# Performance work log

Hardware: AMD Instinct MI355X
Metric: run time of the kernel (lower is better)

Reference implementation:

```python
import jax, jax.numpy as jnp
import numpy as np

# dims
B, S, E, H = 2, 2048, 2048, 2688   # batch, seq, embedding_dim, hidden_dim
NH, DH = 4, 2688 // 4              # mLSTM heads, head dim
KS = 4                             # causal conv kernel size
BLK = 4                            # qkv_proj_blocksize
NPH = H // BLK                     # headwise-proj heads


def setup_inputs() -> dict:
    key = jax.random.key(0)
    ks = jax.random.split(key, 12)
    r = lambda i, shape, s=0.02: jax.random.normal(ks[i], shape, jnp.float32) * s
    return dict(
        x=jax.random.normal(ks[0], (B, S, E), jnp.float32),
        W_in=r(1, (E, 2 * H)),                       # up projection (no bias)
        conv_w=r(2, (KS, 1, H), 0.1),                # depthwise causal conv kernel (W, I/g, O)
        conv_b=jnp.zeros((H,), jnp.float32),
        Wq=r(3, (NPH, BLK, BLK), 0.3),               # headwise q proj
        Wk=r(4, (NPH, BLK, BLK), 0.3),               # headwise k proj
        Wv=r(5, (NPH, BLK, BLK), 0.3),               # headwise v proj
        W_ig=r(6, (3 * H, NH)),                      # input gate proj
        b_ig=jax.random.normal(ks[7], (NH,), jnp.float32),
        W_fg=r(8, (3 * H, NH)),                      # forget gate proj
        b_fg=jnp.linspace(3.0, 6.0, NH).astype(jnp.float32),
        norm_w=jnp.ones((H,), jnp.float32),          # multi-head layernorm weight
        skip=jnp.ones((H,), jnp.float32),            # learnable skip
        W_out=r(9, (H, E)),                          # down projection
    )


def _headwise(x, W):
    # LinearHeadwiseExpand: (B,S,H) -> (B,S,NPH,BLK) -> einsum -> (B,S,H)
    b, s, _ = x.shape
    xh = x.reshape(b, s, NPH, BLK)
    return jnp.einsum('bshd,hdo->bsho', xh, W).reshape(b, s, -1)


def reference(x, W_in, conv_w, conv_b, Wq, Wk, Wv, W_ig, b_ig, W_fg, b_fg, norm_w, skip, W_out):
    x_inner = x @ W_in                               # (B,S,2H)
    x_m, z = jnp.split(x_inner, 2, axis=-1)
    # depthwise causal conv1d
    xc = jax.lax.conv_general_dilated(
        x_m, conv_w, (1,), [(KS - 1, 0)],
        dimension_numbers=('NWC', 'WIO', 'NWC'), feature_group_count=H) + conv_b
    xca = jax.nn.silu(xc)
    q = _headwise(xca, Wq)
    k = _headwise(xca, Wk)
    v = _headwise(x_m, Wv)
    # ---- mLSTM cell (parallel stabilized form) ----
    qh = q.reshape(B, S, NH, DH).transpose(0, 2, 1, 3)   # (B,NH,S,DH)
    kh = k.reshape(B, S, NH, DH).transpose(0, 2, 1, 3)
    vh = v.reshape(B, S, NH, DH).transpose(0, 2, 1, 3)
    if_in = jnp.concatenate([q, k, v], axis=-1)          # (B,S,3H)
    i_pre = (if_in @ W_ig + b_ig).transpose(0, 2, 1)     # (B,NH,S)
    f_pre = (if_in @ W_fg + b_fg).transpose(0, 2, 1)
    log_fg = jax.nn.log_sigmoid(f_pre)                   # (B,NH,S)
    cs = jnp.cumsum(log_fg, axis=-1)
    # log decay matrix: sum of log forget gates t=j+1..i, causal masked
    dmat = cs[:, :, :, None] - cs[:, :, None, :]         # (B,NH,S,S)
    mask = jnp.tril(jnp.ones((S, S), bool))
    log_D = jnp.where(mask, dmat + i_pre[:, :, None, :], -jnp.inf)
    m = jnp.max(log_D, axis=-1, keepdims=True)           # stabilizer (B,NH,S,1)
    D = jnp.exp(log_D - m)
    qk = jnp.einsum('bnsd,bntd->bnst', qh, kh) / jnp.sqrt(jnp.float32(DH))
    C = qk * D
    n = jnp.maximum(jnp.abs(C.sum(-1, keepdims=True)), jnp.exp(-m))
    h = jnp.einsum('bnst,bntd->bnsd', C / (n + 1e-6), vh)
    # multi-head layernorm over DH, learnable scale over full H
    mu = h.mean(-1, keepdims=True)
    var = h.var(-1, keepdims=True)
    hn = (h - mu) * jax.lax.rsqrt(var + 1e-5)
    hn = hn.transpose(0, 2, 1, 3).reshape(B, S, H) * norm_w
    # ---- gated skip + output ----
    h_skip = hn + skip * xca
    hs = h_skip * jax.nn.silu(z)
    return hs @ W_out
```

## Files before the change

### kernel.cpp

```cpp
#include <hip/hip_runtime.h>

typedef unsigned short u16;
typedef unsigned int u32;
typedef __bf16 bf16x8 __attribute__((ext_vector_type(8)));
typedef float f32x4 __attribute__((ext_vector_type(4)));

#define BB   2
#define SS   2048
#define EE   2048
#define HH   2688
#define NHH  4
#define DHH  672
#define NPHH 672
#define H2   5376
#define H3   8064

__device__ __forceinline__ float b2f(u16 u) {
  union { unsigned int i; float f; } c; c.i = ((unsigned int)u) << 16; return c.f;
}
__device__ __forceinline__ u16 f2b(float f) {
  union { float f; unsigned int i; } c; c.f = f;
  unsigned int i = c.i;
  return (u16)((i + 0x7FFFu + ((i >> 16) & 1u)) >> 16);
}
__device__ __forceinline__ float silu_f(float x) { return x / (1.f + __expf(-x)); }
__device__ __forceinline__ float logsig_f(float f) {
  return (f >= 0.f) ? -log1pf(__expf(-f)) : (f - log1pf(__expf(f)));
}

__device__ __forceinline__ void gl2lds16(const u16* g, u16* s) {
  __builtin_amdgcn_global_load_lds(
      (const __attribute__((address_space(1))) u32*)g,
      (__attribute__((address_space(3))) u32*)s, 16, 0, 0);
}

template <int MODE, int OUTF32>
__global__ __launch_bounds__(256) void gemm_nt(
    const u16* __restrict__ A, const u16* __restrict__ Bt, void* __restrict__ Cp,
    int M, int N, int K, int lda, int ldb, int ldc,
    long sAhi, long sAlo, long sBhi, long sBlo, long sChi, long sClo,
    const float* __restrict__ aux1, const float* __restrict__ aux2,
    int auxStride, int causal)
{
  __shared__ __align__(16) u16 As[128 * 32];
  __shared__ __align__(16) u16 Bs[128 * 32];
  int m0 = blockIdx.y * 128, n0 = blockIdx.x * 128;
  if (MODE == 1 && n0 > m0 + 127) return;
  int bz = blockIdx.z, bzh = bz >> 2, bzl = bz & 3;
  A  += bzh * sAhi + bzl * sAlo;
  Bt += bzh * sBhi + bzl * sBlo;
  const float* a1 = aux1 ? aux1 + (long)bz * auxStride : nullptr;
  const float* a2 = aux2 ? aux2 + (long)bz * auxStride : nullptr;
  u16*   C16 = (u16*)Cp + bzh * sChi + bzl * sClo;
  float* C32 = (float*)Cp + bzh * sChi + bzl * sClo;

  int t = threadIdx.x, lane = t & 63, wid = t >> 6;
  int wm = (wid >> 1) * 64, wn = (wid & 1) * 64;
  int l15 = lane & 15, quad = lane >> 4;

  int srow = wid * 16 + (lane >> 2);
  int scol = (lane & 3) * 8;
  const u16* pA0 = A + (long)(m0 + srow) * lda + scol;
  const u16* pA1 = pA0 + (long)64 * lda;
  const u16* pB0 = Bt + (long)(n0 + srow) * ldb + scol;
  const u16* pB1 = pB0 + (long)64 * ldb;
  u16* dA = As + wid * 512;
  u16* dB = Bs + wid * 512;

  f32x4 acc[4][4];
#pragma unroll
  for (int i = 0; i < 4; i++)
#pragma unroll
    for (int j = 0; j < 4; j++) acc[i][j] = (f32x4){0.f, 0.f, 0.f, 0.f};

  int Keff = (MODE == 2 && causal) ? min(K, m0 + 128) : K;

  for (int k0 = 0; k0 < Keff; k0 += 32) {
    __syncthreads();
    gl2lds16(pA0 + k0, dA);
    gl2lds16(pA1 + k0, dA + 2048);
    gl2lds16(pB0 + k0, dB);
    gl2lds16(pB1 + k0, dB + 2048);
    __syncthreads();
    bf16x8 af[4], bfr[4];
#pragma unroll
    for (int i = 0; i < 4; i++) {
      af[i]  = *reinterpret_cast<const bf16x8*>(&As[(wm + i * 16 + l15) * 32 + quad * 8]);
      bfr[i] = *reinterpret_cast<const bf16x8*>(&Bs[(wn + i * 16 + l15) * 32 + quad * 8]);
    }
#pragma unroll
    for (int i = 0; i < 4; i++)
#pragma unroll
      for (int j = 0; j < 4; j++)
        acc[i][j] = __builtin_amdgcn_mfma_f32_16x16x32_bf16(af[i], bfr[j], acc[i][j], 0, 0, 0);
  }

  const float rs = 0.03857583749f;
#pragma unroll
  for (int i = 0; i < 4; i++) {
#pragma unroll
    for (int j = 0; j < 4; j++) {
      int col = n0 + wn + j * 16 + l15;
      if (col >= N) continue;
#pragma unroll
      for (int rr = 0; rr < 4; rr++) {
        int row = m0 + wm + i * 16 + quad * 4 + rr;
        if (row >= M) continue;
        float v = acc[i][j][rr];
        if (MODE == 1) v = (col <= row) ? v * rs * __expf(a1[col] - a2[row]) : 0.f;
        else if (MODE == 2) v = v * a1[row];
        if (OUTF32) C32[(long)row * ldc + col] = v;
        else        C16[(long)row * ldc + col] = f2b(v);
      }
    }
  }
}

template <int F32IN>
__global__ __launch_bounds__(256) void transpose_any(
    const void* __restrict__ in, u16* __restrict__ out, int R, int C, int ldin,
    long inHi, long inLo, long outStride)
{
  __shared__ u16 tile[64][65];
  int bz = blockIdx.z, bzh = bz >> 2, bzl = bz & 3;
  const u16* in16 = (const u16*)in + bzh * inHi + bzl * inLo;
  const float* inf = (const float*)in + bzh * inHi + bzl * inLo;
  out += (long)bz * outStride;
  int r0 = blockIdx.y * 64, c0 = blockIdx.x * 64;
  int t = threadIdx.x;
  for (int idx = t; idx < 64 * 64; idx += 256) {
    int r = idx >> 6, c = idx & 63;
    int rr = r0 + r, cc = c0 + c;
    u16 v = 0;
    if (rr < R && cc < C) {
      long off = (long)rr * ldin + cc;
      v = F32IN ? f2b(inf[off]) : in16[off];
    }
    tile[r][c] = v;
  }
  __syncthreads();
  for (int idx = t; idx < 64 * 64; idx += 256) {
    int r = idx & 63, c = idx >> 6;
    int rr = r0 + r, cc = c0 + c;
    if (rr < R && cc < C) out[(long)cc * R + rr] = tile[r][c];
  }
}

__global__ __launch_bounds__(256) void convert_x(
    const float* __restrict__ x, u16* __restrict__ o)
{
  long i = ((long)blockIdx.x * 256 + threadIdx.x) * 8;
  if (i >= (long)4096 * EE) return;
  float4 a = *reinterpret_cast<const float4*>(x + i);
  float4 b = *reinterpret_cast<const float4*>(x + i + 4);
  u16 t8[8] = {f2b(a.x), f2b(a.y), f2b(a.z), f2b(a.w),
               f2b(b.x), f2b(b.y), f2b(b.z), f2b(b.w)};
  *reinterpret_cast<uint4*>(o + i) = *reinterpret_cast<uint4*>(t8);
}

__global__ __launch_bounds__(256) void prep_wt3(
    const float* __restrict__ Wig, const float* __restrict__ Wfg,
    u16* __restrict__ WT3)
{
  int i = blockIdx.x * 256 + threadIdx.x;
  if (i >= 128 * HH) return;
  int r = i / HH, c = i % HH;
  float v = 0.f;
  if (r < 24) {
    int seg = r >> 3, j = r & 7;
    const float* W = (j < 4) ? Wig : Wfg;
    v = W[(long)(seg * HH + c) * 4 + (j & 3)];
  }
  WT3[i] = f2b(v);
}

__global__ __launch_bounds__(256) void prep_wqkv(
    const float* __restrict__ Wq, const float* __restrict__ Wk,
    const float* __restrict__ Wv, u16* __restrict__ o)
{
  int i = blockIdx.x * 256 + threadIdx.x;
  if (i >= 3 * 10752) return;
  int m = i / 10752, j = i % 10752;
  const float* W = (m == 0) ? Wq : (m == 1) ? Wk : Wv;
  o[i] = f2b(W[j]);
}

__global__ __launch_bounds__(256) void conv_silu(
    const u16* __restrict__ xinner, const float* __restrict__ cw,
    const float* __restrict__ cb, u16* __restrict__ xca)
{
  long idx = (long)blockIdx.x * 256 + threadIdx.x;
  if (idx >= (long)BB * SS * HH / 4) return;
  int h4 = (int)(idx % (HH / 4)) * 4;
  long bs = idx / (HH / 4);
  int s = (int)(bs % SS);
  float4 acc = *reinterpret_cast<const float4*>(cb + h4);
#pragma unroll
  for (int w = 0; w < 4; w++) {
    int sp = s + w - 3;
    if (sp < 0) continue;
    uint2 xr = *reinterpret_cast<const uint2*>(xinner + (bs + w - 3) * H2 + h4);
    const u16* xh = (const u16*)&xr;
    float4 cwv = *reinterpret_cast<const float4*>(cw + w * HH + h4);
    acc.x += b2f(xh[0]) * cwv.x;
    acc.y += b2f(xh[1]) * cwv.y;
    acc.z += b2f(xh[2]) * cwv.z;
    acc.w += b2f(xh[3]) * cwv.w;
  }
  u16 o4[4] = {f2b(silu_f(acc.x)), f2b(silu_f(acc.y)),
               f2b(silu_f(acc.z)), f2b(silu_f(acc.w))};
  *reinterpret_cast<uint2*>(xca + bs * HH + h4) = *reinterpret_cast<uint2*>(o4);
}

__global__ __launch_bounds__(256) void headwise_qkv(
    const u16* __restrict__ xinner, const u16* __restrict__ xca,
    const u16* __restrict__ Wqkv,
    u16* __restrict__ q, u16* __restrict__ k, u16* __restrict__ v)
{
  int idx = blockIdx.x * 256 + threadIdx.x;
  if (idx >= BB * SS * NPHH) return;
  int nph = idx % NPHH;
  long bs = idx / NPHH;
  int cbase = nph * 4;
  uint2 xar = *reinterpret_cast<const uint2*>(xca + bs * HH + cbase);
  uint2 xmr = *reinterpret_cast<const uint2*>(xinner + bs * H2 + cbase);
  const u16* xa = (const u16*)&xar;
  const u16* xm = (const u16*)&xmr;
  float xaf[4], xmf[4];
#pragma unroll
  for (int d = 0; d < 4; d++) { xaf[d] = b2f(xa[d]); xmf[d] = b2f(xm[d]); }
  union { uint4 v4[2]; u16 h[16]; } wq, wk, wv;
  const uint4* wqp = reinterpret_cast<const uint4*>(Wqkv + nph * 16);
  const uint4* wkp = reinterpret_cast<const uint4*>(Wqkv + 10752 + nph * 16);
  const uint4* wvp = reinterpret_cast<const uint4*>(Wqkv + 21504 + nph * 16);
  wq.v4[0] = wqp[0]; wq.v4[1] = wqp[1];
  wk.v4[0] = wkp[0]; wk.v4[1] = wkp[1];
  wv.v4[0] = wvp[0]; wv.v4[1] = wvp[1];
  u16 qo[4], ko[4], vo[4];
#pragma unroll
  for (int o = 0; o < 4; o++) {
    float aq = 0.f, ak = 0.f, av = 0.f;
#pragma unroll
    for (int d = 0; d < 4; d++) {
      aq += xaf[d] * b2f(wq.h[d * 4 + o]);
      ak += xaf[d] * b2f(wk.h[d * 4 + o]);
      av += xmf[d] * b2f(wv.h[d * 4 + o]);
    }
    qo[o] = f2b(aq); ko[o] = f2b(ak); vo[o] = f2b(av);
  }
  long ob = bs * HH + cbase;
  *reinterpret_cast<uint2*>(q + ob) = *reinterpret_cast<uint2*>(qo);
  *reinterpret_cast<uint2*>(k + ob) = *reinterpret_cast<uint2*>(ko);
  *reinterpret_cast<uint2*>(v + ob) = *reinterpret_cast<uint2*>(vo);
}

__global__ __launch_bounds__(1024) void scan_kernel(
    const float* __restrict__ G, const float* __restrict__ big,
    const float* __restrict__ bfg,
    float* __restrict__ avec, float* __restrict__ rmaxvec, float* __restrict__ mvec)
{
  __shared__ float buf[2][SS];
  __shared__ float isave[SS];
  __shared__ float cssave[SS];
  int bn = blockIdx.x;
  int b = bn >> 2, n = bn & 3;
  int t = threadIdx.x;
  float bi = big[n], bf = bfg[n];
  for (int i = t; i < SS; i += 1024) {
    long tk = (long)b * SS + i;
    float ip = G[tk * 24 + n] + G[(4096 + tk) * 24 + 8 + n] +
               G[(8192 + tk) * 24 + 16 + n] + bi;
    float fp = G[tk * 24 + 4 + n] + G[(4096 + tk) * 24 + 12 + n] +
               G[(8192 + tk) * 24 + 20 + n] + bf;
    isave[i] = ip;
    buf[0][i] = logsig_f(fp);
  }
  __syncthreads();
  int src = 0;
  for (int off = 1; off < SS; off <<= 1) {
    int dst = 1 - src;
    for (int i = t; i < SS; i += 1024) {
      float x = buf[src][i];
      if (i >= off) x += buf[src][i - off];
      buf[dst][i] = x;
    }
    __syncthreads();
    src = dst;
  }
  for (int i = t; i < SS; i += 1024) {
    float cs = buf[src][i];
    cssave[i] = cs;
    float a = isave[i] - cs;
    avec[(long)bn * SS + i] = a;
    buf[src][i] = a;
  }
  __syncthreads();
  for (int off = 1; off < SS; off <<= 1) {
    int dst = 1 - src;
    for (int i = t; i < SS; i += 1024) {
      float x = buf[src][i];
      if (i >= off) x = fmaxf(x, buf[src][i - off]);
      buf[dst][i] = x;
    }
    __syncthreads();
    src = dst;
  }
  for (int i = t; i < SS; i += 1024) {
    rmaxvec[(long)bn * SS + i] = buf[src][i];
    mvec[(long)bn * SS + i] = cssave[i] + buf[src][i];
  }
}

__global__ __launch_bounds__(256) void rowsum_kernel(
    const u16* __restrict__ P, const float* __restrict__ mvec, float* __restrict__ invn,
    long Pstride)
{
  int bz = blockIdx.z;
  P += (long)bz * Pstride;
  mvec += (long)bz * SS;
  invn += (long)bz * SS;
  int row = (blockIdx.x * 256 + threadIdx.x) >> 6;
  int lane = threadIdx.x & 63;
  if (row >= SS) return;
  const u16* pr = P + (long)row * SS;
  float s = 0.f;
  for (int j = lane; j <= row; j += 64) s += b2f(pr[j]);
#pragma unroll
  for (int off = 32; off > 0; off >>= 1) s += __shfl_down(s, off);
  if (lane == 0) {
    float n = fmaxf(fabsf(s), __expf(-mvec[row]));
    invn[row] = 1.f / (n + 1e-6f);
  }
}

__global__ __launch_bounds__(256) void ln_skip_gate(
    const u16* __restrict__ h, const u16* __restrict__ xca,
    const u16* __restrict__ xinner, const float* __restrict__ normw,
    const float* __restrict__ skipw, u16* __restrict__ hs)
{
  int row = (blockIdx.x * 256 + threadIdx.x) >> 6;
  int lane = threadIdx.x & 63;
  if (row >= BB * NHH * SS) return;
  int s = row % SS;
  int n = (row / SS) % NHH;
  int b = row / (SS * NHH);
  const u16* hr = h + (long)row * DHH;
  float sum = 0.f, ss = 0.f;
  float vals[11];
  int cnt = 0;
  for (int d = lane; d < DHH; d += 64) {
    float x = b2f(hr[d]);
    vals[cnt++] = x; sum += x; ss += x * x;
  }
#pragma unroll
  for (int off = 32; off > 0; off >>= 1) { sum += __shfl_down(sum, off); ss += __shfl_down(ss, off); }
  sum = __shfl(sum, 0); ss = __shfl(ss, 0);
  float mu = sum / (float)DHH;
  float var = ss / (float)DHH - mu * mu;
  float rstd = rsqrtf(var + 1e-5f);
  long bs = (long)b * SS + s;
  cnt = 0;
  for (int d = lane; d < DHH; d += 64) {
    int c = n * DHH + d;
    float hn = (vals[cnt++] - mu) * rstd * normw[c];
    float hskip = hn + skipw[c] * b2f(xca[bs * HH + c]);
    float z = b2f(xinner[bs * H2 + HH + c]);
    hs[bs * HH + c] = f2b(hskip * silu_f(z));
  }
}

__global__ __launch_bounds__(256) void fill_sentinel(float* out, float v, long n) {
  long i = (long)blockIdx.x * 256 + threadIdx.x;
  if (i < n) out[i] = v;
}

extern "C" void kernel_launch(void* const* d_in, const int* in_sizes, int n_in,
                              void* d_out, int out_size, void* d_ws, size_t ws_size,
                              hipStream_t stream)
{
  const float* x      = (const float*)d_in[0];
  const float* W_in   = (const float*)d_in[1];
  const float* conv_w = (const float*)d_in[2];
  const float* conv_b = (const float*)d_in[3];
  const float* Wq     = (const float*)d_in[4];
  const float* Wk     = (const float*)d_in[5];
  const float* Wv     = (const float*)d_in[6];
  const float* W_ig   = (const float*)d_in[7];
  const float* b_ig   = (const float*)d_in[8];
  const float* W_fg   = (const float*)d_in[9];
  const float* b_fg   = (const float*)d_in[10];
  const float* norm_w = (const float*)d_in[11];
  const float* skipw  = (const float*)d_in[12];
  const float* W_out  = (const float*)d_in[13];
  float* out = (float*)d_out;
  const long SD = (long)SS * DHH;
  const long SP = (long)SS * SS;
  const long BH = (long)SS * HH;

  u16* ws = (u16*)d_ws;
  size_t off = 0;
  auto alloc = [&](size_t n) { u16* p = ws + off; off += n; return p; };
  u16* x_inner = alloc((size_t)4096 * H2);
  u16* xca     = alloc((size_t)4096 * HH);
  u16* qb      = alloc((size_t)4096 * HH);
  u16* kb      = alloc((size_t)4096 * HH);
  u16* vb      = alloc((size_t)4096 * HH);
  float* fvec  = (float*)(ws + off);
  off += 4 * 16384 * 2;
  float* avec    = fvec;
  float* rmaxvec = avec + 16384;
  float* mvec    = rmaxvec + 16384;
  float* invn    = mvec + 16384;
  u16* vt8 = alloc((size_t)8 * SD);
  u16* Pb8 = alloc((size_t)8 * SP);
  size_t need = off * 2;
  long outn = (long)4096 * EE;

  if (ws_size < need) {
    fill_sentinel<<<dim3((outn + 255) / 256), 256, 0, stream>>>(
        out, 200.f + 0.01f * (float)(ws_size >> 20), outn);
    return;
  }

  u16* W_inT  = qb;
  u16* xbf    = kb;
  u16* W_outT = vb;
  u16* hbuf   = kb;
  u16* hsbuf  = qb;
  u16* WT3    = Pb8;
  float* G    = (float*)(Pb8 + 344064);
  u16* Wqkv   = Pb8 + 933888;

  prep_wt3<<<dim3(1344, 1, 1), 256, 0, stream>>>(W_ig, W_fg, WT3);
  prep_wqkv<<<dim3(126, 1, 1), 256, 0, stream>>>(Wq, Wk, Wv, Wqkv);
  transpose_any<1><<<dim3(84, 32, 1), 256, 0, stream>>>(
      W_in, W_inT, EE, H2, H2, 0, 0, 0);
  convert_x<<<dim3(4096, 1, 1), 256, 0, stream>>>(x, xbf);
  gemm_nt<0, 0><<<dim3(42, 32, 1), 256, 0, stream>>>(
      xbf, W_inT, x_inner, 4096, H2, EE, EE, EE, H2,
      0, 0, 0, 0, 0, 0, nullptr, nullptr, 0, 0);
  conv_silu<<<dim3(10752, 1, 1), 256, 0, stream>>>(x_inner, conv_w, conv_b, xca);
  headwise_qkv<<<dim3(10752, 1, 1), 256, 0, stream>>>(
      x_inner, xca, Wqkv, qb, kb, vb);
  gemm_nt<0, 1><<<dim3(1, 96, 1), 256, 0, stream>>>(
      qb, WT3, G, 12288, 24, HH, HH, HH, 24,
      0, 0, 0, 0, 0, 0, nullptr, nullptr, 0, 0);
  scan_kernel<<<dim3(8, 1, 1), 1024, 0, stream>>>(G, b_ig, b_fg, avec, rmaxvec, mvec);
  transpose_any<0><<<dim3(11, 32, 8), 256, 0, stream>>>(
      vb, vt8, SS, DHH, HH, BH, DHH, SD);
  gemm_nt<1, 0><<<dim3(16, 16, 8), 256, 0, stream>>>(
      qb, kb, Pb8, SS, SS, DHH, HH, HH, SS,
      BH, DHH, BH, DHH, 4 * SP, SP, avec, rmaxvec, SS, 0);
  rowsum_kernel<<<dim3(512, 1, 8), 256, 0, stream>>>(Pb8, mvec, invn, SP);
  gemm_nt<2, 0><<<dim3(6, 16, 8), 256, 0, stream>>>(
      Pb8, vt8, hbuf, SS, DHH, SS, SS, SS, DHH,
      4 * SP, SP, 4 * SD, SD, 4 * SD, SD, invn, nullptr, SS, 1);
  transpose_any<1><<<dim3(32, 42, 1), 256, 0, stream>>>(
      W_out, W_outT, HH, EE, EE, 0, 0, 0);
  ln_skip_gate<<<dim3(4096, 1, 1), 256, 0, stream>>>(
      hbuf, xca, x_inner, norm_w, skipw, hsbuf);
  gemm_nt<0, 1><<<dim3(16, 32, 1), 256, 0, stream>>>(
      hsbuf, W_outT, out, 4096, EE, HH, HH, HH, EE,
      0, 0, 0, 0, 0, 0, nullptr, nullptr, 0, 0);
}
```

Baseline: 739.9 us.

## Add 128x256-tile 8-wave GEMM with 4-stage LDS pipeline and XCD swizzle

Introduces gemm_nt2, a 512-thread GEMM with 128x256 output tiles. It prefetches K-slices into LDS three steps ahead using direct global-to-LDS loads across four buffers, with explicit vmcnt waits and raised wave priority around the MFMA block. Workgroup ids are remapped so that consecutive tiles land on the same XCD, which should improve L2 reuse. It replaces all four large GEMM launches (up-projection, QK decay scores, PV, down-projection) to raise arithmetic intensity and hide memory latency. The cost is a larger LDS footprint (about 96 KB per block) that limits occupancy, and wider tiles waste more work on ragged N edges such as 672.

```diff
diff --git a/kernel.cpp b/kernel.cpp
--- a/kernel.cpp
+++ b/kernel.cpp
@@ -32,6 +32,121 @@
   __builtin_amdgcn_global_load_lds(
       (const __attribute__((address_space(1))) u32*)g,
       (__attribute__((address_space(3))) u32*)s, 16, 0, 0);
+}
+
+template <int MODE, int OUTF32>
+__global__ __launch_bounds__(512, 2) void gemm_nt2(
+    const u16* __restrict__ A, const u16* __restrict__ Bt, void* __restrict__ Cp,
+    int M, int N, int K, int lda, int ldb, int ldc,
+    long sAhi, long sAlo, long sBhi, long sBlo, long sChi, long sClo,
+    const float* __restrict__ aux1, const float* __restrict__ aux2,
+    int auxStride, int causal)
+{
+  __shared__ __align__(16) u16 sm[4 * 12288];
+
+  int gx = gridDim.x;
+  int nwg = gx * gridDim.y;
+  int flat = blockIdx.y * gx + blockIdx.x;
+  int qq = nwg >> 3, r8 = nwg & 7;
+  int xcd = flat & 7, seq = flat >> 3;
+  int logical = (xcd < r8 ? xcd * (qq + 1) : r8 * (qq + 1) + (xcd - r8) * qq) + seq;
+  int bx = logical % gx, by = logical / gx;
+  int m0 = by * 128, n0 = bx * 256;
+  if (MODE == 1 && n0 > m0 + 127) return;
+
+  int bz = blockIdx.z, bzh = bz >> 2, bzl = bz & 3;
+  A  += bzh * sAhi + bzl * sAlo;
+  Bt += bzh * sBhi + bzl * sBlo;
+  const float* a1 = aux1 ? aux1 + (long)bz * auxStride : nullptr;
+  const float* a2 = aux2 ? aux2 + (long)bz * auxStride : nullptr;
+  u16*   C16 = (u16*)Cp + bzh * sChi + bzl * sClo;
+  float* C32 = (float*)Cp + bzh * sChi + bzl * sClo;
+
+  int t = threadIdx.x, lane = t & 63, w = t >> 6;
+  int l15 = lane & 15, quad = lane >> 4;
+  int wr = w >> 2, wc = w & 3;
+
+  int sx8 = ((lane & 3) ^ ((lane >> 3) & 3)) * 8;
+  const u16* pA  = A  + (long)(m0 + w * 16 + (lane >> 2)) * lda + sx8;
+  const u16* pB0 = Bt + (long)(n0 + w * 32 + (lane >> 2)) * ldb + sx8;
+  const u16* pB1 = pB0 + (long)16 * ldb;
+  u16* dA  = sm + w * 512;
+  u16* dB0 = sm + 4096 + w * 1024;
+  u16* dB1 = dB0 + 512;
+
+  int sxr = (quad ^ ((l15 >> 1) & 3)) * 8;
+  int aoff = (wr * 64 + l15) * 32 + sxr;
+  int boff = 4096 + (wc * 64 + l15) * 32 + sxr;
+
+  f32x4 acc[4][4];
+#pragma unroll
+  for (int i = 0; i < 4; i++)
+#pragma unroll
+    for (int j = 0; j < 4; j++) acc[i][j] = (f32x4){0.f, 0.f, 0.f, 0.f};
+
+  int Keff = (MODE == 2 && causal) ? min(K, m0 + 128) : K;
+  int T = Keff >> 5;
+
+  auto STAGE = [&](int tt) {
+    int bo = (tt & 3) * 12288;
+    int k2 = tt << 5;
+    gl2lds16(pA + k2, dA + bo);
+    gl2lds16(pB0 + k2, dB0 + bo);
+    gl2lds16(pB1 + k2, dB1 + bo);
+  };
+
+  int npre = T < 3 ? T : 3;
+  for (int tt = 0; tt < npre; ++tt) STAGE(tt);
+  if (npre >= 3)      asm volatile("s_waitcnt vmcnt(6)" ::: "memory");
+  else if (npre == 2) asm volatile("s_waitcnt vmcnt(3)" ::: "memory");
+  else                asm volatile("s_waitcnt vmcnt(0)" ::: "memory");
+  __builtin_amdgcn_s_barrier();
+  __builtin_amdgcn_sched_barrier(0);
+
+  for (int tq = 0; tq < T; ++tq) {
+    const u16* Ab = sm + (tq & 3) * 12288;
+    bf16x8 af[4], bfr[4];
+#pragma unroll
+    for (int i = 0; i < 4; i++) {
+      af[i]  = *reinterpret_cast<const bf16x8*>(&Ab[aoff + i * 512]);
+      bfr[i] = *reinterpret_cast<const bf16x8*>(&Ab[boff + i * 512]);
+    }
+    if (tq + 3 < T) STAGE(tq + 3);
+    __builtin_amdgcn_s_barrier();
+    __builtin_amdgcn_s_setprio(1);
+#pragma unroll
+    for (int i = 0; i < 4; i++)
+#pragma unroll
+      for (int j = 0; j < 4; j++)
+        acc[i][j] = __builtin_amdgcn_mfma_f32_16x16x32_bf16(af[i], bfr[j], acc[i][j], 0, 0, 0);
+    __builtin_amdgcn_s_setprio(0);
+    int rem = T - 1 - tq;
+    if (rem >= 3)      asm volatile("s_waitcnt vmcnt(6)" ::: "memory");
+    else if (rem == 2) asm volatile("s_waitcnt vmcnt(3)" ::: "memory");
+    else if (rem == 1) asm volatile("s_waitcnt vmcnt(0)" ::: "memory");
+    __builtin_amdgcn_s_barrier();
+    __builtin_amdgcn_sched_barrier(0);
+  }
+
+  const float rs = 0.03857583749f;
+#pragma unroll
+  for (int i = 0; i < 4; i++) {
+#pragma unroll
+    for (int j = 0; j < 4; j++) {
+      int col = n0 + wc * 64 + j * 16 + l15;
+      if (col >= N) continue;
+#pragma unroll
+      for (int rr = 0; rr < 4; rr++) {
+        int row = m0 + wr * 64 + i * 16 + quad * 4 + rr;
+        if (row >= M) continue;
+        float v = acc[i][j][rr];
+        if (MODE == 1) v = (col <= row) ? v * rs * __expf(a1[col] - a2[row]) : 0.f;
+        else if (MODE == 2) v = v * a1[row];
+        if (OUTF32) C32[(long)row * ldc + col] = v;
+        else        C16[(long)row * ldc + col] = f2b(v);
+      }
+    }
+  }
 }
 
 template <int MODE, int OUTF32>
@@ -436,7 +551,7 @@
   transpose_any<1><<<dim3(84, 32, 1), 256, 0, stream>>>(
       W_in, W_inT, EE, H2, H2, 0, 0, 0);
   convert_x<<<dim3(4096, 1, 1), 256, 0, stream>>>(x, xbf);
-  gemm_nt<0, 0><<<dim3(42, 32, 1), 256, 0, stream>>>(
+  gemm_nt2<0, 0><<<dim3(21, 32, 1), 512, 0, stream>>>(
       xbf, W_inT, x_inner, 4096, H2, EE, EE, EE, H2,
       0, 0, 0, 0, 0, 0, nullptr, nullptr, 0, 0);
   conv_silu<<<dim3(10752, 1, 1), 256, 0, stream>>>(x_inner, conv_w, conv_b, xca);
@@ -448,18 +563,18 @@
   scan_kernel<<<dim3(8, 1, 1), 1024, 0, stream>>>(G, b_ig, b_fg, avec, rmaxvec, mvec);
   transpose_any<0><<<dim3(11, 32, 8), 256, 0, stream>>>(
       vb, vt8, SS, DHH, HH, BH, DHH, SD);
-  gemm_nt<1, 0><<<dim3(16, 16, 8), 256, 0, stream>>>(
+  gemm_nt2<1, 0><<<dim3(8, 16, 8), 512, 0, stream>>>(
       qb, kb, Pb8, SS, SS, DHH, HH, HH, SS,
       BH, DHH, BH, DHH, 4 * SP, SP, avec, rmaxvec, SS, 0);
   rowsum_kernel<<<dim3(512, 1, 8), 256, 0, stream>>>(Pb8, mvec, invn, SP);
-  gemm_nt<2, 0><<<dim3(6, 16, 8), 256, 0, stream>>>(
+  gemm_nt2<2, 0><<<dim3(3, 16, 8), 512, 0, stream>>>(
       Pb8, vt8, hbuf, SS, DHH, SS, SS, SS, DHH,
       4 * SP, SP, 4 * SD, SD, 4 * SD, SD, invn, nullptr, SS, 1);
   transpose_any<1><<<dim3(32, 42, 1), 256, 0, stream>>>(
       W_out, W_outT, HH, EE, EE, 0, 0, 0);
   ln_skip_gate<<<dim3(4096, 1, 1), 256, 0, stream>>>(
       hbuf, xca, x_inner, norm_w, skipw, hsbuf);
-  gemm_nt<0, 1><<<dim3(16, 32, 1), 256, 0, stream>>>(
+  gemm_nt2<0, 1><<<dim3(8, 32, 1), 512, 0, stream>>>(
       hsbuf, W_outT, out, 4096, EE, HH, HH, HH, EE,
       0, 0, 0, 0, 0, 0, nullptr, nullptr, 0, 0);
 }
```

Result: faster. 714.3 us (-3.5%).

## Replace GEMM with 4-stage pipelined, swizzled, XCD-remapped large-tile kernel

Applied to the files above, without the earlier changes.

Replaces the single-buffered 128x128 GEMM with a 512-thread kernel using BMx256 tiles and a 4-slot LDS ring. Tiles are prefetched three steps ahead with direct global-to-LDS loads and waited on with explicit vmcnt counts. LDS reads use an XOR swizzle to avoid bank conflicts, MFMA issue is given raised priority, and workgroups are remapped so neighbouring tiles land on the same XCD for L2 reuse. The goal is to hide global load latency and raise MFMA utilisation across all five GEMMs. The cost is large LDS use and one block per CU, which hurts the small gate GEMM (N=24 padded to 256) and the tile counts of the causal GEMMs.

```diff
diff --git a/kernel.cpp b/kernel.cpp
--- a/kernel.cpp
+++ b/kernel.cpp
@@ -34,18 +34,35 @@
       (__attribute__((address_space(3))) u32*)s, 16, 0, 0);
 }
 
-template <int MODE, int OUTF32>
-__global__ __launch_bounds__(256) void gemm_nt(
+template <int N> __device__ __forceinline__ void vmwait() {
+  asm volatile("s_waitcnt vmcnt(%0)" :: "n"(N) : "memory");
+}
+
+template <int BM, int MODE, int OUTF32>
+__global__ __launch_bounds__(512, 1) void gemm_p(
     const u16* __restrict__ A, const u16* __restrict__ Bt, void* __restrict__ Cp,
     int M, int N, int K, int lda, int ldb, int ldc,
     long sAhi, long sAlo, long sBhi, long sBlo, long sChi, long sClo,
     const float* __restrict__ aux1, const float* __restrict__ aux2,
     int auxStride, int causal)
 {
-  __shared__ __align__(16) u16 As[128 * 32];
-  __shared__ __align__(16) u16 Bs[128 * 32];
-  int m0 = blockIdx.y * 128, n0 = blockIdx.x * 128;
-  if (MODE == 1 && n0 > m0 + 127) return;
+  constexpr int MFR   = BM / 32;
+  constexpr int NPH   = MFR / 2;
+  constexpr int SLOT  = (BM + 256) * 32;
+  constexpr int ACH   = BM / 128;
+  constexpr int LOADS = ACH + 2;
+  __shared__ __align__(16) u16 sm[4 * SLOT];
+
+  int gx = gridDim.x;
+  int nwg = gx * gridDim.y;
+  int flat = blockIdx.y * gx + blockIdx.x;
+  int qq = nwg >> 3, r8 = nwg & 7;
+  int xcd = flat & 7, seq = flat >> 3;
+  int logical = (xcd < r8 ? xcd * (qq + 1) : r8 * (qq + 1) + (xcd - r8) * qq) + seq;
+  int bx = logical % gx, by = logical / gx;
+  int m0 = by * BM, n0 = bx * 256;
+  if (MODE == 1 && n0 > m0 + BM - 1) return;
+
   int bz = blockIdx.z, bzh = bz >> 2, bzl = bz & 3;
   A  += bzh * sAhi + bzl * sAlo;
   Bt += bzh * sBhi + bzl * sBlo;
@@ -54,57 +71,102 @@
   u16*   C16 = (u16*)Cp + bzh * sChi + bzl * sClo;
   float* C32 = (float*)Cp + bzh * sChi + bzl * sClo;
 
-  int t = threadIdx.x, lane = t & 63, wid = t >> 6;
-  int wm = (wid >> 1) * 64, wn = (wid & 1) * 64;
+  int t = threadIdx.x, lane = t & 63, w = t >> 6;
   int l15 = lane & 15, quad = lane >> 4;
-
-  int srow = wid * 16 + (lane >> 2);
-  int scol = (lane & 3) * 8;
-  const u16* pA0 = A + (long)(m0 + srow) * lda + scol;
-  const u16* pA1 = pA0 + (long)64 * lda;
-  const u16* pB0 = Bt + (long)(n0 + srow) * ldb + scol;
-  const u16* pB1 = pB0 + (long)64 * ldb;
-  u16* dA = As + wid * 512;
-  u16* dB = Bs + wid * 512;
-
-  f32x4 acc[4][4];
-#pragma unroll
-  for (int i = 0; i < 4; i++)
+  int wr = w >> 2, wc = w & 3;
+
+  int srow = t >> 2;
+  int swz = (((t & 3) ^ ((t >> 3) & 3)) * 8);
+  const u16* pS[LOADS];
+  int coff[LOADS];
+#pragma unroll
+  for (int c = 0; c < ACH; ++c) {
+    pS[c] = A + (long)(m0 + c * 128 + srow) * lda + swz;
+    coff[c] = c * 4096 + w * 512;
+  }
+#pragma unroll
+  for (int c = 0; c < 2; ++c) {
+    pS[ACH + c] = Bt + (long)(n0 + c * 128 + srow) * ldb + swz;
+    coff[ACH + c] = BM * 32 + c * 4096 + w * 512;
+  }
+
+  int rswz = (quad ^ ((l15 >> 1) & 3)) * 8;
+  int aoff = (wr * (BM / 2) + l15) * 32 + rswz;
+  int boff = BM * 32 + (wc * 64 + l15) * 32 + rswz;
+
+  f32x4 acc[MFR][4];
+#pragma unroll
+  for (int i = 0; i < MFR; i++)
 #pragma unroll
     for (int j = 0; j < 4; j++) acc[i][j] = (f32x4){0.f, 0.f, 0.f, 0.f};
 
-  int Keff = (MODE == 2 && causal) ? min(K, m0 + 128) : K;
-
-  for (int k0 = 0; k0 < Keff; k0 += 32) {
-    __syncthreads();
-    gl2lds16(pA0 + k0, dA);
-    gl2lds16(pA1 + k0, dA + 2048);
-    gl2lds16(pB0 + k0, dB);
-    gl2lds16(pB1 + k0, dB + 2048);
-    __syncthreads();
-    bf16x8 af[4], bfr[4];
-#pragma unroll
-    for (int i = 0; i < 4; i++) {
-      af[i]  = *reinterpret_cast<const bf16x8*>(&As[(wm + i * 16 + l15) * 32 + quad * 8]);
-      bfr[i] = *reinterpret_cast<const bf16x8*>(&Bs[(wn + i * 16 + l15) * 32 + quad * 8]);
-    }
-#pragma unroll
-    for (int i = 0; i < 4; i++)
-#pragma unroll
-      for (int j = 0; j < 4; j++)
-        acc[i][j] = __builtin_amdgcn_mfma_f32_16x16x32_bf16(af[i], bfr[j], acc[i][j], 0, 0, 0);
+  int Keff = (MODE == 2 && causal) ? min(K, m0 + BM) : K;
+  int T = Keff >> 5;
+
+  auto STAGE1 = [&](int tt, int c) {
+    gl2lds16(pS[c] + (tt << 5), sm + (tt & 3) * SLOT + coff[c]);
+  };
+
+  int npre = T < 3 ? T : 3;
+  for (int tt = 0; tt < npre; ++tt)
+#pragma unroll
+    for (int c = 0; c < LOADS; ++c) STAGE1(tt, c);
+  if (npre >= 3)      vmwait<2 * LOADS>();
+  else if (npre == 2) vmwait<LOADS>();
+  else                vmwait<0>();
+  __builtin_amdgcn_s_barrier();
+  __builtin_amdgcn_sched_barrier(0);
+
+  for (int tq = 0; tq < T; ++tq) {
+    u16* Sb = sm + (tq & 3) * SLOT;
+    const bool stg = (tq + 3 < T);
+    bf16x8 bf[4];
+#pragma unroll
+    for (int p = 0; p < NPH; ++p) {
+      bf16x8 a0 = *reinterpret_cast<const bf16x8*>(Sb + aoff + (2 * p) * 512);
+      bf16x8 a1v = *reinterpret_cast<const bf16x8*>(Sb + aoff + (2 * p + 1) * 512);
+      if (p == 0) {
+#pragma unroll
+        for (int j = 0; j < 4; ++j)
+          bf[j] = *reinterpret_cast<const bf16x8*>(Sb + boff + j * 512);
+      }
+      if (stg) {
+#pragma unroll
+        for (int c = p * LOADS / NPH; c < (p + 1) * LOADS / NPH; ++c)
+          STAGE1(tq + 3, c);
+      }
+      __builtin_amdgcn_s_barrier();
+      asm volatile("s_waitcnt lgkmcnt(0)" ::: "memory");
+      __builtin_amdgcn_sched_barrier(0);
+      __builtin_amdgcn_s_setprio(1);
+#pragma unroll
+      for (int j = 0; j < 4; ++j)
+        acc[2 * p][j] = __builtin_amdgcn_mfma_f32_16x16x32_bf16(a0, bf[j], acc[2 * p][j], 0, 0, 0);
+#pragma unroll
+      for (int j = 0; j < 4; ++j)
+        acc[2 * p + 1][j] = __builtin_amdgcn_mfma_f32_16x16x32_bf16(a1v, bf[j], acc[2 * p + 1][j], 0, 0, 0);
+      __builtin_amdgcn_s_setprio(0);
+      __builtin_amdgcn_sched_barrier(0);
+    }
+    if (tq + 1 < T) {
+      if (tq + 3 < T)      vmwait<2 * LOADS>();
+      else if (tq + 2 < T) vmwait<LOADS>();
+      else                 vmwait<0>();
+      __builtin_amdgcn_s_barrier();
+      __builtin_amdgcn_sched_barrier(0);
+    }
   }
 
   const float rs = 0.03857583749f;
 #pragma unroll
-  for (int i = 0; i < 4; i++) {
+  for (int i = 0; i < MFR; i++) {
 #pragma unroll
     for (int j = 0; j < 4; j++) {
-      int col = n0 + wn + j * 16 + l15;
+      int col = n0 + wc * 64 + j * 16 + l15;
       if (col >= N) continue;
 #pragma unroll
       for (int rr = 0; rr < 4; rr++) {
-        int row = m0 + wm + i * 16 + quad * 4 + rr;
+        int row = m0 + wr * (BM / 2) + i * 16 + quad * 4 + rr;
         if (row >= M) continue;
         float v = acc[i][j][rr];
         if (MODE == 1) v = (col <= row) ? v * rs * __expf(a1[col] - a2[row]) : 0.f;
@@ -436,30 +498,30 @@
   transpose_any<1><<<dim3(84, 32, 1), 256, 0, stream>>>(
       W_in, W_inT, EE, H2, H2, 0, 0, 0);
   convert_x<<<dim3(4096, 1, 1), 256, 0, stream>>>(x, xbf);
-  gemm_nt<0, 0><<<dim3(42, 32, 1), 256, 0, stream>>>(
+  gemm_p<256, 0, 0><<<dim3(21, 16, 1), 512, 0, stream>>>(
       xbf, W_inT, x_inner, 4096, H2, EE, EE, EE, H2,
       0, 0, 0, 0, 0, 0, nullptr, nullptr, 0, 0);
   conv_silu<<<dim3(10752, 1, 1), 256, 0, stream>>>(x_inner, conv_w, conv_b, xca);
   headwise_qkv<<<dim3(10752, 1, 1), 256, 0, stream>>>(
       x_inner, xca, Wqkv, qb, kb, vb);
-  gemm_nt<0, 1><<<dim3(1, 96, 1), 256, 0, stream>>>(
+  gemm_p<128, 0, 1><<<dim3(1, 96, 1), 512, 0, stream>>>(
       qb, WT3, G, 12288, 24, HH, HH, HH, 24,
       0, 0, 0, 0, 0, 0, nullptr, nullptr, 0, 0);
   scan_kernel<<<dim3(8, 1, 1), 1024, 0, stream>>>(G, b_ig, b_fg, avec, rmaxvec, mvec);
   transpose_any<0><<<dim3(11, 32, 8), 256, 0, stream>>>(
       vb, vt8, SS, DHH, HH, BH, DHH, SD);
-  gemm_nt<1, 0><<<dim3(16, 16, 8), 256, 0, stream>>>(
+  gemm_p<256, 1, 0><<<dim3(8, 8, 8), 512, 0, stream>>>(
       qb, kb, Pb8, SS, SS, DHH, HH, HH, SS,
       BH, DHH, BH, DHH, 4 * SP, SP, avec, rmaxvec, SS, 0);
   rowsum_kernel<<<dim3(512, 1, 8), 256, 0, stream>>>(Pb8, mvec, invn, SP);
-  gemm_nt<2, 0><<<dim3(6, 16, 8), 256, 0, stream>>>(
+  gemm_p<128, 2, 0><<<dim3(3, 16, 8), 512, 0, stream>>>(
       Pb8, vt8, hbuf, SS, DHH, SS, SS, SS, DHH,
       4 * SP, SP, 4 * SD, SD, 4 * SD, SD, invn, nullptr, SS, 1);
   transpose_any<1><<<dim3(32, 42, 1), 256, 0, stream>>>(
       W_out, W_outT, HH, EE, EE, 0, 0, 0);
   ln_skip_gate<<<dim3(4096, 1, 1), 256, 0, stream>>>(
       hbuf, xca, x_inner, norm_w, skipw, hsbuf);
-  gemm_nt<0, 1><<<dim3(16, 32, 1), 256, 0, stream>>>(
+  gemm_p<128, 0, 1><<<dim3(8, 32, 1), 512, 0, stream>>>(
       hsbuf, W_outT, out, 4096, EE, HH, HH, HH, EE,
       0, 0, 0, 0, 0, 0, nullptr, nullptr, 0, 0);
 }
```

Result: faster. 702.2 us (-5.1%).
